# Kernel optimization log

Measured on AMD Instinct MI355X. Metric: run time of the kernel, lower is better.

## Reference

```python
import jax, jax.numpy as jnp
import numpy as np

B = 16384
IN = 512
H = 512

def setup_inputs() -> dict:
    key = jax.random.key(0)
    ks = jax.random.split(key, 8)
    inp = {
        "x_t": jax.random.normal(ks[0], (B, IN), dtype=jnp.float32),
        "h_t": jax.random.normal(ks[1], (B, H), dtype=jnp.float32),
        "W_ir": jax.random.normal(ks[2], (IN, H), dtype=jnp.float32),
        "W_hr": jax.random.normal(ks[3], (H, H), dtype=jnp.float32),
        "b_r": jnp.zeros((H,), dtype=jnp.float32),
        "W_iz": jax.random.normal(ks[4], (IN, H), dtype=jnp.float32),
        "W_hz": jax.random.normal(ks[5], (H, H), dtype=jnp.float32),
        "b_z": jnp.zeros((H,), dtype=jnp.float32),
        "W_in": jax.random.normal(ks[6], (IN, H), dtype=jnp.float32),
        "W_hn": jax.random.normal(ks[7], (H, H), dtype=jnp.float32),
        "b_n": jnp.zeros((H,), dtype=jnp.float32),
    }
    return inp

def reference(x_t, h_t, W_ir, W_hr, b_r, W_iz, W_hz, b_z, W_in, W_hn, b_n):
    # Fuse the three input-side and three hidden-side GEMMs by concatenating weights.
    Wi = jnp.concatenate([W_ir, W_iz, W_in], axis=1)   # [IN, 3H]
    Wh = jnp.concatenate([W_hr, W_hz, W_hn], axis=1)   # [H, 3H]
    gi = x_t @ Wi                                      # [B, 3H]
    gh = h_t @ Wh                                      # [B, 3H]
    h = b_r.shape[0]
    r_t = jax.nn.sigmoid(gi[:, :h] + gh[:, :h] + b_r)
    z_t = jax.nn.sigmoid(gi[:, h:2*h] + gh[:, h:2*h] + b_z)
    n_t = jnp.tanh(gi[:, 2*h:] + r_t * gh[:, 2*h:] + b_n)
    return (1.0 - z_t) * n_t + z_t * h_t
```

## Files before the change

### kernel.cpp

```cpp
#include <hip/hip_runtime.h>
#include <hip/hip_fp16.h>

typedef _Float16 half8 __attribute__((ext_vector_type(8)));
typedef float floatx4 __attribute__((ext_vector_type(4)));

#define AS1 __attribute__((address_space(1)))
#define AS3 __attribute__((address_space(3)))

#define WTOT ((size_t)(8 * 16 * 12 * 2048))
#define APERM_OFF WTOT
#define APERM_HALFS ((size_t)128 * 16 * 4 * 4096)
#define WLO_OFF (6 * 512 * 512)
#define WMAT_STRIDE ((size_t)(8 * 16 * 2048))

__device__ __forceinline__ void async_lds16(const void* g, void* l) {
  __builtin_amdgcn_global_load_lds((const AS1 void*)g, (AS3 void*)l, 16, 0, 0);
}

__global__ __launch_bounds__(256) void prep(
    const float* __restrict__ x, const float* __restrict__ h,
    const float* __restrict__ Wir, const float* __restrict__ Whr,
    const float* __restrict__ Wiz, const float* __restrict__ Whz,
    const float* __restrict__ Win, const float* __restrict__ Whn,
    _Float16* __restrict__ wperm) {
  __shared__ __align__(16) float xt[128 * 36];
  __shared__ __align__(16) float ht[128 * 36];
  const int b = blockIdx.x;
  const int t = threadIdx.x;

  if (b >= 2048) {
    const int b2 = b - 2048;
    const int w = b2 >> 7;
    const int rem = b2 & 127;
    const int ki = rem >> 3;
    const int nt = rem & 7;
    const float* W = (w == 0) ? Wir : (w == 1) ? Whr : (w == 2) ? Wiz
                   : (w == 3) ? Whz : (w == 4) ? Win : Whn;
    const int k0 = ki * 32, n0 = nt * 64;
    const int kk = t >> 3;
    const int nn = (t & 7) * 8;
    const float* src = W + (k0 + kk) * 512 + n0 + nn;
    float4 f0 = *(const float4*)(src);
    float4 f1 = *(const float4*)(src + 4);
    float* drow = xt + kk * 68 + nn;
    *(float4*)(drow) = f0;
    *(float4*)(drow + 4) = f1;
    __syncthreads();
    const int u = t >> 6, l = t & 63;
    const int nloc = 16 * u + (l & 15);
    const int kbase = 8 * (l >> 4);
    half8 vh2, vl2;
#pragma unroll
    for (int j = 0; j < 8; ++j) {
      float f = xt[(kbase + j) * 68 + nloc];
      _Float16 hi = (_Float16)f;
      _Float16 lo = (_Float16)(f - (float)hi);
      vh2[j] = hi;
      vl2[j] = lo;
    }
    const size_t base = ((size_t)((nt * 16 + ki) * 12)) * 2048 + t * 8;
    *(half8*)(wperm + base + (size_t)w * 2048) = vh2;
    *(half8*)(wperm + base + (size_t)(6 + w) * 2048) = vl2;
    return;
  }

  const int mt = b >> 4, kt = b & 15;
  const float* xb = x + ((size_t)(mt * 128)) * 512 + kt * 32;
  const float* hb = h + ((size_t)(mt * 128)) * 512 + kt * 32;
#pragma unroll
  for (int p = 0; p < 2; ++p) {
    const int r = (t >> 2) + p * 64;
    const int c = (t & 3) * 8;
    const float* sx = xb + (size_t)r * 512 + c;
    const float* sh = hb + (size_t)r * 512 + c;
    float4 a0 = *(const float4*)(sx);
    float4 a1 = *(const float4*)(sx + 4);
    float4 b0 = *(const float4*)(sh);
    float4 b1 = *(const float4*)(sh + 4);
    *(float4*)(xt + r * 36 + c) = a0;
    *(float4*)(xt + r * 36 + c + 4) = a1;
    *(float4*)(ht + r * 36 + c) = b0;
    *(float4*)(ht + r * 36 + c + 4) = b1;
  }
  __syncthreads();
  _Float16* dst = wperm + APERM_OFF + ((size_t)(mt * 16 + kt)) * 16384;
#pragma unroll
  for (int hc = 0; hc < 2; ++hc) {
    const int cc = t + hc * 256;
    const int m = 16 * (cc >> 6) + (cc & 15);
    const int kA = 8 * ((cc >> 4) & 3);
    half8 xh, xl, hh, hl;
#pragma unroll
    for (int j = 0; j < 8; ++j) {
      float fx = xt[m * 36 + kA + j];
      float fh = ht[m * 36 + kA + j];
      _Float16 a = (_Float16)fx;
      xh[j] = a; xl[j] = (_Float16)(fx - (float)a);
      _Float16 bb = (_Float16)fh;
      hh[j] = bb; hl[j] = (_Float16)(fh - (float)bb);
    }
    *(half8*)(dst + 0 * 4096 + cc * 8) = xh;
    *(half8*)(dst + 1 * 4096 + cc * 8) = xl;
    *(half8*)(dst + 2 * 4096 + cc * 8) = hh;
    *(half8*)(dst + 3 * 4096 + cc * 8) = hl;
  }
}

__global__ __launch_bounds__(512, 4) void gru_fused3(
    const float* __restrict__ h, const _Float16* __restrict__ wperm,
    const float* __restrict__ br, const float* __restrict__ bz,
    const float* __restrict__ bn, float* __restrict__ out) {
  __shared__ __align__(16) _Float16 ldsA[2 * 4 * 4096];

  const int t = threadIdx.x;
  const int lane = t & 63;
  const int wv = t >> 6;
  const int wm = wv >> 2;
  const int wn = wv & 3;
  const int bid = blockIdx.x;
  const int xcd = bid & 7;
  const int g = bid >> 3;
  const int nt = g & 7;
  const int mt = (g >> 3) * 8 + xcd;
  const int m0 = mt * 128;
  const int n0 = nt * 64;
  const _Float16* aperm = wperm + APERM_OFF + (size_t)mt * 16 * 16384;

  floatx4 acc_r[4] = {};
  floatx4 acc_z[4] = {};
  floatx4 acc_in[4] = {};
  floatx4 acc_hn[4] = {};

  const int soff = (wv >> 1) * 4096 + (wv & 1) * 2048 + lane * 8;

  {
    const _Float16* asrc = aperm + soff;
    _Float16* adst = ldsA + soff;
#pragma unroll
    for (int q = 0; q < 4; ++q) async_lds16(asrc + q * 512, adst + q * 512);
  }
  __syncthreads();

#pragma unroll 2
  for (int kt = 0; kt < 16; ++kt) {
    const _Float16* A = ldsA + (kt & 1) * 16384;
    const _Float16* wb = wperm + ((size_t)((nt * 16 + kt) * 12)) * 2048
                         + wn * 512 + lane * 8;

    half8 bh0 = *(const half8*)(wb + (size_t)0 * 2048);
    half8 bh1 = *(const half8*)(wb + (size_t)1 * 2048);
    half8 bh2 = *(const half8*)(wb + (size_t)2 * 2048);
    half8 bh3 = *(const half8*)(wb + (size_t)3 * 2048);
    half8 bh4 = *(const half8*)(wb + (size_t)4 * 2048);
    half8 bh5 = *(const half8*)(wb + (size_t)5 * 2048);
    __builtin_amdgcn_sched_barrier(0);

    if (kt < 15) {
      const _Float16* asrc = aperm + (size_t)(kt + 1) * 16384 + soff;
      _Float16* adst = ldsA + ((kt & 1) ^ 1) * 16384 + soff;
#pragma unroll
      for (int q = 0; q < 4; ++q) async_lds16(asrc + q * 512, adst + q * 512);
    }
    __builtin_amdgcn_sched_barrier(0);

    __builtin_amdgcn_s_setprio(1);
#pragma unroll
    for (int i = 0; i < 4; ++i) {
      const int ao = (((wm << 2) + i) * 64 + lane) * 8;
      half8 axh = *(const half8*)(A + 0 * 4096 + ao);
      half8 axl = *(const half8*)(A + 1 * 4096 + ao);
      acc_r[i]  = __builtin_amdgcn_mfma_f32_16x16x32_f16(axh, bh0, acc_r[i], 0, 0, 0);
      acc_z[i]  = __builtin_amdgcn_mfma_f32_16x16x32_f16(axh, bh2, acc_z[i], 0, 0, 0);
      acc_in[i] = __builtin_amdgcn_mfma_f32_16x16x32_f16(axh, bh4, acc_in[i], 0, 0, 0);
      acc_r[i]  = __builtin_amdgcn_mfma_f32_16x16x32_f16(axl, bh0, acc_r[i], 0, 0, 0);
      acc_z[i]  = __builtin_amdgcn_mfma_f32_16x16x32_f16(axl, bh2, acc_z[i], 0, 0, 0);
      acc_in[i] = __builtin_amdgcn_mfma_f32_16x16x32_f16(axl, bh4, acc_in[i], 0, 0, 0);
      half8 ahh = *(const half8*)(A + 2 * 4096 + ao);
      half8 ahl = *(const half8*)(A + 3 * 4096 + ao);
      acc_r[i]  = __builtin_amdgcn_mfma_f32_16x16x32_f16(ahh, bh1, acc_r[i], 0, 0, 0);
      acc_z[i]  = __builtin_amdgcn_mfma_f32_16x16x32_f16(ahh, bh3, acc_z[i], 0, 0, 0);
      acc_hn[i] = __builtin_amdgcn_mfma_f32_16x16x32_f16(ahh, bh5, acc_hn[i], 0, 0, 0);
      acc_r[i]  = __builtin_amdgcn_mfma_f32_16x16x32_f16(ahl, bh1, acc_r[i], 0, 0, 0);
      acc_z[i]  = __builtin_amdgcn_mfma_f32_16x16x32_f16(ahl, bh3, acc_z[i], 0, 0, 0);
      acc_hn[i] = __builtin_amdgcn_mfma_f32_16x16x32_f16(ahl, bh5, acc_hn[i], 0, 0, 0);
    }
    __builtin_amdgcn_s_setprio(0);
    __builtin_amdgcn_sched_barrier(0);

    half8 bl0 = *(const half8*)(wb + (size_t)6 * 2048);
    half8 bl1 = *(const half8*)(wb + (size_t)7 * 2048);
    half8 bl2 = *(const half8*)(wb + (size_t)8 * 2048);
    half8 bl3 = *(const half8*)(wb + (size_t)9 * 2048);
    half8 bl4 = *(const half8*)(wb + (size_t)10 * 2048);
    half8 bl5 = *(const half8*)(wb + (size_t)11 * 2048);
    __builtin_amdgcn_sched_barrier(0);

    __builtin_amdgcn_s_setprio(1);
#pragma unroll
    for (int i = 0; i < 4; ++i) {
      const int ao = (((wm << 2) + i) * 64 + lane) * 8;
      half8 axh = *(const half8*)(A + 0 * 4096 + ao);
      acc_r[i]  = __builtin_amdgcn_mfma_f32_16x16x32_f16(axh, bl0, acc_r[i], 0, 0, 0);
      acc_z[i]  = __builtin_amdgcn_mfma_f32_16x16x32_f16(axh, bl2, acc_z[i], 0, 0, 0);
      acc_in[i] = __builtin_amdgcn_mfma_f32_16x16x32_f16(axh, bl4, acc_in[i], 0, 0, 0);
      half8 ahh = *(const half8*)(A + 2 * 4096 + ao);
      acc_r[i]  = __builtin_amdgcn_mfma_f32_16x16x32_f16(ahh, bl1, acc_r[i], 0, 0, 0);
      acc_z[i]  = __builtin_amdgcn_mfma_f32_16x16x32_f16(ahh, bl3, acc_z[i], 0, 0, 0);
      acc_hn[i] = __builtin_amdgcn_mfma_f32_16x16x32_f16(ahh, bl5, acc_hn[i], 0, 0, 0);
    }
    __builtin_amdgcn_s_setprio(0);

    __syncthreads();
  }

  const int quad = lane >> 4;
  const int col = lane & 15;
  const int n = n0 + wn * 16 + col;
  const float vbr = br[n], vbz = bz[n], vbn = bn[n];
#pragma unroll
  for (int i = 0; i < 4; ++i) {
    const int mbase = m0 + wm * 64 + i * 16 + quad * 4;
#pragma unroll
    for (int r = 0; r < 4; ++r) {
      const int m = mbase + r;
      const float gr = acc_r[i][r] + vbr;
      const float gz = acc_z[i][r] + vbz;
      const float rg = 1.0f / (1.0f + __expf(-gr));
      const float zg = 1.0f / (1.0f + __expf(-gz));
      const float gn = acc_in[i][r] + rg * acc_hn[i][r] + vbn;
      const float e2 = __expf(2.0f * gn);
      const float ntv = 1.0f - 2.0f / (e2 + 1.0f);
      const float hp = h[m * 512 + n];
      out[m * 512 + n] = (1.0f - zg) * ntv + zg * hp;
    }
  }
}

__global__ __launch_bounds__(256) void permute_w_old(
    const float* __restrict__ Wir, const float* __restrict__ Whr,
    const float* __restrict__ Wiz, const float* __restrict__ Whz,
    const float* __restrict__ Win, const float* __restrict__ Whn,
    _Float16* __restrict__ wperm) {
  __shared__ __align__(16) float tile[32 * 68];
  const int b = blockIdx.x;
  const int t = threadIdx.x;
  const int w = b >> 7;
  const int rem = b & 127;
  const int ki = rem >> 3;
  const int nt = rem & 7;
  const float* W = (w == 0) ? Wir : (w == 1) ? Whr : (w == 2) ? Wiz
                 : (w == 3) ? Whz : (w == 4) ? Win : Whn;
  const int k0 = ki * 32, n0 = nt * 64;
  const int kk = t >> 3;
  const int nn = (t & 7) * 8;
  const float* src = W + (k0 + kk) * 512 + n0 + nn;
  float4 f0 = *(const float4*)(src);
  float4 f1 = *(const float4*)(src + 4);
  float* drow = tile + kk * 68 + nn;
  *(float4*)(drow) = f0;
  *(float4*)(drow + 4) = f1;
  __syncthreads();
  const int u = t >> 6, l = t & 63;
  const int nloc = 16 * u + (l & 15);
  const int kbase = 8 * (l >> 4);
  half8 vh2, vl2;
#pragma unroll
  for (int j = 0; j < 8; ++j) {
    float f = tile[(kbase + j) * 68 + nloc];
    _Float16 hi = (_Float16)f;
    _Float16 lo = (_Float16)(f - (float)hi);
    vh2[j] = hi;
    vl2[j] = lo;
  }
  const size_t off = ((size_t)((w * 8 + nt) * 16 + ki)) * 2048 + t * 8;
  *(half8*)(wperm + off) = vh2;
  *(half8*)(wperm + WLO_OFF + off) = vl2;
}

__global__ __launch_bounds__(256, 2) void gru_fused_fb(
    const float* __restrict__ x, const float* __restrict__ h,
    const _Float16* __restrict__ wperm,
    const float* __restrict__ br, const float* __restrict__ bz,
    const float* __restrict__ bn, float* __restrict__ out) {
  __shared__ __align__(16) _Float16 ldsA[2 * 4 * 4096];
  const int t = threadIdx.x;
  const int lane = t & 63;
  const int wn = t >> 6;
  const int bid = blockIdx.x;
  const int nt = bid & 7;
  const int mt = bid >> 3;
  const int m0 = mt * 128;
  const int n0 = nt * 64;
  const _Float16* wlo = wperm + WLO_OFF;

  floatx4 acc_r[8] = {};
  floatx4 acc_z[8] = {};
  floatx4 acc_in[8] = {};
  floatx4 acc_hn[8] = {};

  const int mA = 16 * (t >> 6) + (t & 15);
  const int kA = 8 * ((t >> 4) & 3);
  const float* px0 = x + (m0 + mA) * 512 + kA;
  const float* ph0 = h + (m0 + mA) * 512 + kA;
  const float* px1 = px0 + 64 * 512;
  const float* ph1 = ph0 + 64 * 512;
  const int c0 = t, c1 = t + 256;

  {
    float v[4][8];
    *(float4*)&v[0][0] = *(const float4*)(px0); *(float4*)&v[0][4] = *(const float4*)(px0 + 4);
    *(float4*)&v[1][0] = *(const float4*)(px1); *(float4*)&v[1][4] = *(const float4*)(px1 + 4);
    *(float4*)&v[2][0] = *(const float4*)(ph0); *(float4*)&v[2][4] = *(const float4*)(ph0 + 4);
    *(float4*)&v[3][0] = *(const float4*)(ph1); *(float4*)&v[3][4] = *(const float4*)(ph1 + 4);
#pragma unroll
    for (int g = 0; g < 4; ++g) {
      half8 hi, lo;
#pragma unroll
      for (int j = 0; j < 8; ++j) {
        _Float16 a = (_Float16)v[g][j];
        hi[j] = a;
        lo[j] = (_Float16)(v[g][j] - (float)a);
      }
      const int c = (g & 1) ? c1 : c0;
      const int part = (g >> 1) * 2;
      *(half8*)(ldsA + (part + 0) * 4096 + c * 8) = hi;
      *(half8*)(ldsA + (part + 1) * 4096 + c * 8) = lo;
    }
  }
  __syncthreads();

#pragma unroll 2
  for (int kt = 0; kt < 16; ++kt) {
    const _Float16* A = ldsA + (kt & 1) * 16384;
    const size_t tb = ((size_t)(nt * 16 + kt)) * 2048 + wn * 512 + lane * 8;
    half8 bh_ir = *(const half8*)(wperm + tb + 0 * WMAT_STRIDE);
    half8 bh_hr = *(const half8*)(wperm + tb + 1 * WMAT_STRIDE);
    half8 bh_iz = *(const half8*)(wperm + tb + 2 * WMAT_STRIDE);
    half8 bh_hz = *(const half8*)(wperm + tb + 3 * WMAT_STRIDE);
    half8 bh_in = *(const half8*)(wperm + tb + 4 * WMAT_STRIDE);
    half8 bh_hn = *(const half8*)(wperm + tb + 5 * WMAT_STRIDE);
    half8 bl_ir = *(const half8*)(wlo + tb + 0 * WMAT_STRIDE);
    half8 bl_hr = *(const half8*)(wlo + tb + 1 * WMAT_STRIDE);
    half8 bl_iz = *(const half8*)(wlo + tb + 2 * WMAT_STRIDE);
    half8 bl_hz = *(const half8*)(wlo + tb + 3 * WMAT_STRIDE);
    half8 bl_in = *(const half8*)(wlo + tb + 4 * WMAT_STRIDE);
    half8 bl_hn = *(const half8*)(wlo + tb + 5 * WMAT_STRIDE);
    __builtin_amdgcn_sched_barrier(0);

    float v[4][8];
    if (kt < 15) {
      const int k0 = (kt + 1) * 32;
      *(float4*)&v[0][0] = *(const float4*)(px0 + k0); *(float4*)&v[0][4] = *(const float4*)(px0 + k0 + 4);
      *(float4*)&v[1][0] = *(const float4*)(px1 + k0); *(float4*)&v[1][4] = *(const float4*)(px1 + k0 + 4);
      *(float4*)&v[2][0] = *(const float4*)(ph0 + k0); *(float4*)&v[2][4] = *(const float4*)(ph0 + k0 + 4);
      *(float4*)&v[3][0] = *(const float4*)(ph1 + k0); *(float4*)&v[3][4] = *(const float4*)(ph1 + k0 + 4);
    }
    __builtin_amdgcn_sched_barrier(0);

    __builtin_amdgcn_s_setprio(1);
#pragma unroll
    for (int i = 0; i < 8; ++i) {
      const int ao = (i * 64 + lane) * 8;
      half8 axh = *(const half8*)(A + 0 * 4096 + ao);
      half8 axl = *(const half8*)(A + 1 * 4096 + ao);
      half8 ahh = *(const half8*)(A + 2 * 4096 + ao);
      half8 ahl = *(const half8*)(A + 3 * 4096 + ao);
      acc_r[i]  = __builtin_amdgcn_mfma_f32_16x16x32_f16(axh, bh_ir, acc_r[i], 0, 0, 0);
      acc_r[i]  = __builtin_amdgcn_mfma_f32_16x16x32_f16(ahh, bh_hr, acc_r[i], 0, 0, 0);
      acc_z[i]  = __builtin_amdgcn_mfma_f32_16x16x32_f16(axh, bh_iz, acc_z[i], 0, 0, 0);
      acc_z[i]  = __builtin_amdgcn_mfma_f32_16x16x32_f16(ahh, bh_hz, acc_z[i], 0, 0, 0);
      acc_in[i] = __builtin_amdgcn_mfma_f32_16x16x32_f16(axh, bh_in, acc_in[i], 0, 0, 0);
      acc_hn[i] = __builtin_amdgcn_mfma_f32_16x16x32_f16(ahh, bh_hn, acc_hn[i], 0, 0, 0);
      acc_r[i]  = __builtin_amdgcn_mfma_f32_16x16x32_f16(axl, bh_ir, acc_r[i], 0, 0, 0);
      acc_r[i]  = __builtin_amdgcn_mfma_f32_16x16x32_f16(ahl, bh_hr, acc_r[i], 0, 0, 0);
      acc_z[i]  = __builtin_amdgcn_mfma_f32_16x16x32_f16(axl, bh_iz, acc_z[i], 0, 0, 0);
      acc_z[i]  = __builtin_amdgcn_mfma_f32_16x16x32_f16(ahl, bh_hz, acc_z[i], 0, 0, 0);
      acc_in[i] = __builtin_amdgcn_mfma_f32_16x16x32_f16(axl, bh_in, acc_in[i], 0, 0, 0);
      acc_hn[i] = __builtin_amdgcn_mfma_f32_16x16x32_f16(ahl, bh_hn, acc_hn[i], 0, 0, 0);
      acc_r[i]  = __builtin_amdgcn_mfma_f32_16x16x32_f16(axh, bl_ir, acc_r[i], 0, 0, 0);
      acc_r[i]  = __builtin_amdgcn_mfma_f32_16x16x32_f16(ahh, bl_hr, acc_r[i], 0, 0, 0);
      acc_z[i]  = __builtin_amdgcn_mfma_f32_16x16x32_f16(axh, bl_iz, acc_z[i], 0, 0, 0);
      acc_z[i]  = __builtin_amdgcn_mfma_f32_16x16x32_f16(ahh, bl_hz, acc_z[i], 0, 0, 0);
      acc_in[i] = __builtin_amdgcn_mfma_f32_16x16x32_f16(axh, bl_in, acc_in[i], 0, 0, 0);
      acc_hn[i] = __builtin_amdgcn_mfma_f32_16x16x32_f16(ahh, bl_hn, acc_hn[i], 0, 0, 0);
    }
    __builtin_amdgcn_s_setprio(0);

    if (kt < 15) {
      _Float16* base = ldsA + ((kt & 1) ^ 1) * 16384;
#pragma unroll
      for (int g = 0; g < 4; ++g) {
        half8 hi, lo;
#pragma unroll
        for (int j = 0; j < 8; ++j) {
          _Float16 a = (_Float16)v[g][j];
          hi[j] = a;
          lo[j] = (_Float16)(v[g][j] - (float)a);
        }
        const int c = (g & 1) ? c1 : c0;
        const int part = (g >> 1) * 2;
        *(half8*)(base + (part + 0) * 4096 + c * 8) = hi;
        *(half8*)(base + (part + 1) * 4096 + c * 8) = lo;
      }
    }
    __syncthreads();
  }

  const int quad = lane >> 4;
  const int col = lane & 15;
  const int n = n0 + wn * 16 + col;
  const float vbr = br[n], vbz = bz[n], vbn = bn[n];
#pragma unroll
  for (int i = 0; i < 8; ++i) {
    const int mbase = m0 + i * 16 + quad * 4;
#pragma unroll
    for (int r = 0; r < 4; ++r) {
      const int m = mbase + r;
      const float gr = acc_r[i][r] + vbr;
      const float gz = acc_z[i][r] + vbz;
      const float rg = 1.0f / (1.0f + __expf(-gr));
      const float zg = 1.0f / (1.0f + __expf(-gz));
      const float gn = acc_in[i][r] + rg * acc_hn[i][r] + vbn;
      const float e2 = __expf(2.0f * gn);
      const float ntv = 1.0f - 2.0f / (e2 + 1.0f);
      const float hp = h[m * 512 + n];
      out[m * 512 + n] = (1.0f - zg) * ntv + zg * hp;
    }
  }
}

extern "C" void kernel_launch(void* const* d_in, const int* in_sizes, int n_in,
                              void* d_out, int out_size, void* d_ws, size_t ws_size,
                              hipStream_t stream) {
  const float* x   = (const float*)d_in[0];
  const float* h   = (const float*)d_in[1];
  const float* Wir = (const float*)d_in[2];
  const float* Whr = (const float*)d_in[3];
  const float* br  = (const float*)d_in[4];
  const float* Wiz = (const float*)d_in[5];
  const float* Whz = (const float*)d_in[6];
  const float* bz  = (const float*)d_in[7];
  const float* Win = (const float*)d_in[8];
  const float* Whn = (const float*)d_in[9];
  const float* bn  = (const float*)d_in[10];
  float* out = (float*)d_out;
  _Float16* wperm = (_Float16*)d_ws;

  const size_t need_bytes = (APERM_OFF + APERM_HALFS) * 2;
  if (ws_size >= need_bytes) {
    prep<<<2816, 256, 0, stream>>>(x, h, Wir, Whr, Wiz, Whz, Win, Whn, wperm);
    gru_fused3<<<1024, 512, 0, stream>>>(h, wperm, br, bz, bn, out);
  } else {
    permute_w_old<<<768, 256, 0, stream>>>(Wir, Whr, Wiz, Whz, Win, Whn, wperm);
    gru_fused_fb<<<1024, 256, 0, stream>>>(x, h, wperm, br, bz, bn, out);
  }
}
```

Before: 280.5 us.

## Use 4-wave GRU blocks with 8 M-subtiles per wave; widen prep tiles

The main GEMM kernel moves from 8 waves (2x4 over M and N) to 4 waves, each covering all 128 rows of the block and one 16-column slice. Each wave now reads 8 A fragments per k-step and does twice the MFMA work per weight fragment, so B-fragment global loads are spread over more compute. The hi and lo weight phases are merged into one loop. The prep kernel now handles two K-tiles (64 columns) per block, halving its block count. The trade-off is double the accumulator registers (128 floats per lane) and fewer waves per block, which may lower occupancy and latency hiding.

Result: faster. 259.3 us (-7.5%).

```diff
diff --git a/kernel.cpp b/kernel.cpp
--- a/kernel.cpp
+++ b/kernel.cpp
@@ -23,13 +23,13 @@
     const float* __restrict__ Wiz, const float* __restrict__ Whz,
     const float* __restrict__ Win, const float* __restrict__ Whn,
     _Float16* __restrict__ wperm) {
-  __shared__ __align__(16) float xt[128 * 36];
-  __shared__ __align__(16) float ht[128 * 36];
+  __shared__ __align__(16) float xt[128 * 68];
+  __shared__ __align__(16) float ht[128 * 68];
   const int b = blockIdx.x;
   const int t = threadIdx.x;
 
-  if (b >= 2048) {
-    const int b2 = b - 2048;
+  if (b >= 1024) {
+    const int b2 = b - 1024;
     const int w = b2 >> 7;
     const int rem = b2 & 127;
     const int ki = rem >> 3;
@@ -64,49 +64,60 @@
     return;
   }
 
-  const int mt = b >> 4, kt = b & 15;
-  const float* xb = x + ((size_t)(mt * 128)) * 512 + kt * 32;
-  const float* hb = h + ((size_t)(mt * 128)) * 512 + kt * 32;
+  const int mt = b >> 3;
+  const int kp = b & 7;
 #pragma unroll
   for (int p = 0; p < 2; ++p) {
     const int r = (t >> 2) + p * 64;
-    const int c = (t & 3) * 8;
-    const float* sx = xb + (size_t)r * 512 + c;
-    const float* sh = hb + (size_t)r * 512 + c;
+    const int c = (t & 3) * 16;
+    const float* sx = x + ((size_t)(mt * 128 + r)) * 512 + kp * 64 + c;
+    const float* sh = h + ((size_t)(mt * 128 + r)) * 512 + kp * 64 + c;
     float4 a0 = *(const float4*)(sx);
     float4 a1 = *(const float4*)(sx + 4);
+    float4 a2 = *(const float4*)(sx + 8);
+    float4 a3 = *(const float4*)(sx + 12);
     float4 b0 = *(const float4*)(sh);
     float4 b1 = *(const float4*)(sh + 4);
-    *(float4*)(xt + r * 36 + c) = a0;
-    *(float4*)(xt + r * 36 + c + 4) = a1;
-    *(float4*)(ht + r * 36 + c) = b0;
-    *(float4*)(ht + r * 36 + c + 4) = b1;
+    float4 b2 = *(const float4*)(sh + 8);
+    float4 b3 = *(const float4*)(sh + 12);
+    float* dx = xt + r * 68 + c;
+    float* dh = ht + r * 68 + c;
+    *(float4*)(dx) = a0; *(float4*)(dx + 4) = a1;
+    *(float4*)(dx + 8) = a2; *(float4*)(dx + 12) = a3;
+    *(float4*)(dh) = b0; *(float4*)(dh + 4) = b1;
+    *(float4*)(dh + 8) = b2; *(float4*)(dh + 12) = b3;
   }
   __syncthreads();
-  _Float16* dst = wperm + APERM_OFF + ((size_t)(mt * 16 + kt)) * 16384;
-#pragma unroll
-  for (int hc = 0; hc < 2; ++hc) {
-    const int cc = t + hc * 256;
-    const int m = 16 * (cc >> 6) + (cc & 15);
-    const int kA = 8 * ((cc >> 4) & 3);
-    half8 xh, xl, hh, hl;
-#pragma unroll
-    for (int j = 0; j < 8; ++j) {
-      float fx = xt[m * 36 + kA + j];
-      float fh = ht[m * 36 + kA + j];
-      _Float16 a = (_Float16)fx;
-      xh[j] = a; xl[j] = (_Float16)(fx - (float)a);
-      _Float16 bb = (_Float16)fh;
-      hh[j] = bb; hl[j] = (_Float16)(fh - (float)bb);
-    }
-    *(half8*)(dst + 0 * 4096 + cc * 8) = xh;
-    *(half8*)(dst + 1 * 4096 + cc * 8) = xl;
-    *(half8*)(dst + 2 * 4096 + cc * 8) = hh;
-    *(half8*)(dst + 3 * 4096 + cc * 8) = hl;
-  }
-}
-
-__global__ __launch_bounds__(512, 4) void gru_fused3(
+
+#pragma unroll
+  for (int ii = 0; ii < 2; ++ii) {
+    const int kt = kp * 2 + ii;
+    const int cb = ii * 32;
+    _Float16* dst = wperm + APERM_OFF + ((size_t)(mt * 16 + kt)) * 16384;
+#pragma unroll
+    for (int hc = 0; hc < 2; ++hc) {
+      const int cc = t + hc * 256;
+      const int m = 16 * (cc >> 6) + (cc & 15);
+      const int kA = 8 * ((cc >> 4) & 3);
+      half8 xh, xl, hh, hl;
+#pragma unroll
+      for (int j = 0; j < 8; ++j) {
+        float fx = xt[m * 68 + cb + kA + j];
+        float fh = ht[m * 68 + cb + kA + j];
+        _Float16 a = (_Float16)fx;
+        xh[j] = a; xl[j] = (_Float16)(fx - (float)a);
+        _Float16 bb = (_Float16)fh;
+        hh[j] = bb; hl[j] = (_Float16)(fh - (float)bb);
+      }
+      *(half8*)(dst + 0 * 4096 + cc * 8) = xh;
+      *(half8*)(dst + 1 * 4096 + cc * 8) = xl;
+      *(half8*)(dst + 2 * 4096 + cc * 8) = hh;
+      *(half8*)(dst + 3 * 4096 + cc * 8) = hl;
+    }
+  }
+}
+
+__global__ __launch_bounds__(256, 2) void gru_fused2(
     const float* __restrict__ h, const _Float16* __restrict__ wperm,
     const float* __restrict__ br, const float* __restrict__ bz,
     const float* __restrict__ bn, float* __restrict__ out) {
@@ -115,8 +126,6 @@
   const int t = threadIdx.x;
   const int lane = t & 63;
   const int wv = t >> 6;
-  const int wm = wv >> 2;
-  const int wn = wv & 3;
   const int bid = blockIdx.x;
   const int xcd = bid & 7;
   const int g = bid >> 3;
@@ -126,18 +135,16 @@
   const int n0 = nt * 64;
   const _Float16* aperm = wperm + APERM_OFF + (size_t)mt * 16 * 16384;
 
-  floatx4 acc_r[4] = {};
-  floatx4 acc_z[4] = {};
-  floatx4 acc_in[4] = {};
-  floatx4 acc_hn[4] = {};
-
-  const int soff = (wv >> 1) * 4096 + (wv & 1) * 2048 + lane * 8;
+  floatx4 acc_r[8] = {};
+  floatx4 acc_z[8] = {};
+  floatx4 acc_in[8] = {};
+  floatx4 acc_hn[8] = {};
 
   {
-    const _Float16* asrc = aperm + soff;
-    _Float16* adst = ldsA + soff;
-#pragma unroll
-    for (int q = 0; q < 4; ++q) async_lds16(asrc + q * 512, adst + q * 512);
+    const _Float16* asrc = aperm + wv * 4096 + lane * 8;
+    _Float16* adst = ldsA + wv * 4096;
+#pragma unroll
+    for (int q = 0; q < 8; ++q) async_lds16(asrc + q * 512, adst + q * 512);
   }
   __syncthreads();
 
@@ -145,7 +152,7 @@
   for (int kt = 0; kt < 16; ++kt) {
     const _Float16* A = ldsA + (kt & 1) * 16384;
     const _Float16* wb = wperm + ((size_t)((nt * 16 + kt) * 12)) * 2048
-                         + wn * 512 + lane * 8;
+                         + wv * 512 + lane * 8;
 
     half8 bh0 = *(const half8*)(wb + (size_t)0 * 2048);
     half8 bh1 = *(const half8*)(wb + (size_t)1 * 2048);
@@ -153,40 +160,6 @@
     half8 bh3 = *(const half8*)(wb + (size_t)3 * 2048);
     half8 bh4 = *(const half8*)(wb + (size_t)4 * 2048);
     half8 bh5 = *(const half8*)(wb + (size_t)5 * 2048);
-    __builtin_amdgcn_sched_barrier(0);
-
-    if (kt < 15) {
-      const _Float16* asrc = aperm + (size_t)(kt + 1) * 16384 + soff;
-      _Float16* adst = ldsA + ((kt & 1) ^ 1) * 16384 + soff;
-#pragma unroll
-      for (int q = 0; q < 4; ++q) async_lds16(asrc + q * 512, adst + q * 512);
-    }
-    __builtin_amdgcn_sched_barrier(0);
-
-    __builtin_amdgcn_s_setprio(1);
-#pragma unroll
-    for (int i = 0; i < 4; ++i) {
-      const int ao = (((wm << 2) + i) * 64 + lane) * 8;
-      half8 axh = *(const half8*)(A + 0 * 4096 + ao);
-      half8 axl = *(const half8*)(A + 1 * 4096 + ao);
-      acc_r[i]  = __builtin_amdgcn_mfma_f32_16x16x32_f16(axh, bh0, acc_r[i], 0, 0, 0);
-      acc_z[i]  = __builtin_amdgcn_mfma_f32_16x16x32_f16(axh, bh2, acc_z[i], 0, 0, 0);
-      acc_in[i] = __builtin_amdgcn_mfma_f32_16x16x32_f16(axh, bh4, acc_in[i], 0, 0, 0);
-      acc_r[i]  = __builtin_amdgcn_mfma_f32_16x16x32_f16(axl, bh0, acc_r[i], 0, 0, 0);
-      acc_z[i]  = __builtin_amdgcn_mfma_f32_16x16x32_f16(axl, bh2, acc_z[i], 0, 0, 0);
-      acc_in[i] = __builtin_amdgcn_mfma_f32_16x16x32_f16(axl, bh4, acc_in[i], 0, 0, 0);
-      half8 ahh = *(const half8*)(A + 2 * 4096 + ao);
-      half8 ahl = *(const half8*)(A + 3 * 4096 + ao);
-      acc_r[i]  = __builtin_amdgcn_mfma_f32_16x16x32_f16(ahh, bh1, acc_r[i], 0, 0, 0);
-      acc_z[i]  = __builtin_amdgcn_mfma_f32_16x16x32_f16(ahh, bh3, acc_z[i], 0, 0, 0);
-      acc_hn[i] = __builtin_amdgcn_mfma_f32_16x16x32_f16(ahh, bh5, acc_hn[i], 0, 0, 0);
-      acc_r[i]  = __builtin_amdgcn_mfma_f32_16x16x32_f16(ahl, bh1, acc_r[i], 0, 0, 0);
-      acc_z[i]  = __builtin_amdgcn_mfma_f32_16x16x32_f16(ahl, bh3, acc_z[i], 0, 0, 0);
-      acc_hn[i] = __builtin_amdgcn_mfma_f32_16x16x32_f16(ahl, bh5, acc_hn[i], 0, 0, 0);
-    }
-    __builtin_amdgcn_s_setprio(0);
-    __builtin_amdgcn_sched_barrier(0);
-
     half8 bl0 = *(const half8*)(wb + (size_t)6 * 2048);
     half8 bl1 = *(const half8*)(wb + (size_t)7 * 2048);
     half8 bl2 = *(const half8*)(wb + (size_t)8 * 2048);
@@ -195,15 +168,38 @@
     half8 bl5 = *(const half8*)(wb + (size_t)11 * 2048);
     __builtin_amdgcn_sched_barrier(0);
 
+    if (kt < 15) {
+      const _Float16* asrc = aperm + (size_t)(kt + 1) * 16384 + wv * 4096
+                             + lane * 8;
+      _Float16* adst = ldsA + ((kt & 1) ^ 1) * 16384 + wv * 4096;
+#pragma unroll
+      for (int q = 0; q < 8; ++q) async_lds16(asrc + q * 512, adst + q * 512);
+    }
+    __builtin_amdgcn_sched_barrier(0);
+
     __builtin_amdgcn_s_setprio(1);
 #pragma unroll
-    for (int i = 0; i < 4; ++i) {
-      const int ao = (((wm << 2) + i) * 64 + lane) * 8;
+    for (int i = 0; i < 8; ++i) {
+      const int ao = (i * 64 + lane) * 8;
       half8 axh = *(const half8*)(A + 0 * 4096 + ao);
+      half8 axl = *(const half8*)(A + 1 * 4096 + ao);
+      half8 ahh = *(const half8*)(A + 2 * 4096 + ao);
+      half8 ahl = *(const half8*)(A + 3 * 4096 + ao);
+      acc_r[i]  = __builtin_amdgcn_mfma_f32_16x16x32_f16(axh, bh0, acc_r[i], 0, 0, 0);
+      acc_z[i]  = __builtin_amdgcn_mfma_f32_16x16x32_f16(axh, bh2, acc_z[i], 0, 0, 0);
+      acc_in[i] = __builtin_amdgcn_mfma_f32_16x16x32_f16(axh, bh4, acc_in[i], 0, 0, 0);
+      acc_r[i]  = __builtin_amdgcn_mfma_f32_16x16x32_f16(axl, bh0, acc_r[i], 0, 0, 0);
+      acc_z[i]  = __builtin_amdgcn_mfma_f32_16x16x32_f16(axl, bh2, acc_z[i], 0, 0, 0);
+      acc_in[i] = __builtin_amdgcn_mfma_f32_16x16x32_f16(axl, bh4, acc_in[i], 0, 0, 0);
+      acc_r[i]  = __builtin_amdgcn_mfma_f32_16x16x32_f16(ahh, bh1, acc_r[i], 0, 0, 0);
+      acc_z[i]  = __builtin_amdgcn_mfma_f32_16x16x32_f16(ahh, bh3, acc_z[i], 0, 0, 0);
+      acc_hn[i] = __builtin_amdgcn_mfma_f32_16x16x32_f16(ahh, bh5, acc_hn[i], 0, 0, 0);
+      acc_r[i]  = __builtin_amdgcn_mfma_f32_16x16x32_f16(ahl, bh1, acc_r[i], 0, 0, 0);
+      acc_z[i]  = __builtin_amdgcn_mfma_f32_16x16x32_f16(ahl, bh3, acc_z[i], 0, 0, 0);
+      acc_hn[i] = __builtin_amdgcn_mfma_f32_16x16x32_f16(ahl, bh5, acc_hn[i], 0, 0, 0);
       acc_r[i]  = __builtin_amdgcn_mfma_f32_16x16x32_f16(axh, bl0, acc_r[i], 0, 0, 0);
       acc_z[i]  = __builtin_amdgcn_mfma_f32_16x16x32_f16(axh, bl2, acc_z[i], 0, 0, 0);
       acc_in[i] = __builtin_amdgcn_mfma_f32_16x16x32_f16(axh, bl4, acc_in[i], 0, 0, 0);
-      half8 ahh = *(const half8*)(A + 2 * 4096 + ao);
       acc_r[i]  = __builtin_amdgcn_mfma_f32_16x16x32_f16(ahh, bl1, acc_r[i], 0, 0, 0);
       acc_z[i]  = __builtin_amdgcn_mfma_f32_16x16x32_f16(ahh, bl3, acc_z[i], 0, 0, 0);
       acc_hn[i] = __builtin_amdgcn_mfma_f32_16x16x32_f16(ahh, bl5, acc_hn[i], 0, 0, 0);
@@ -215,11 +211,11 @@
 
   const int quad = lane >> 4;
   const int col = lane & 15;
-  const int n = n0 + wn * 16 + col;
+  const int n = n0 + wv * 16 + col;
   const float vbr = br[n], vbz = bz[n], vbn = bn[n];
 #pragma unroll
-  for (int i = 0; i < 4; ++i) {
-    const int mbase = m0 + wm * 64 + i * 16 + quad * 4;
+  for (int i = 0; i < 8; ++i) {
+    const int mbase = m0 + i * 16 + quad * 4;
 #pragma unroll
     for (int r = 0; r < 4; ++r) {
       const int m = mbase + r;
@@ -448,8 +444,8 @@
 
   const size_t need_bytes = (APERM_OFF + APERM_HALFS) * 2;
   if (ws_size >= need_bytes) {
-    prep<<<2816, 256, 0, stream>>>(x, h, Wir, Whr, Wiz, Whz, Win, Whn, wperm);
-    gru_fused3<<<1024, 512, 0, stream>>>(h, wperm, br, bz, bn, out);
+    prep<<<1792, 256, 0, stream>>>(x, h, Wir, Whr, Wiz, Whz, Win, Whn, wperm);
+    gru_fused2<<<1024, 256, 0, stream>>>(h, wperm, br, bz, bn, out);
   } else {
     permute_w_old<<<768, 256, 0, stream>>>(Wir, Whr, Wiz, Whz, Win, Whn, wperm);
     gru_fused_fb<<<1024, 256, 0, stream>>>(x, h, wperm, br, bz, bn, out);
```
